# Kernel tuning notes

Measured on AMD Instinct MI355X. Metric: run time of the kernel, lower is better.

The kernel has to match this reference:

```python
import jax, jax.numpy as jnp
import numpy as np

B, C_IN, H, W = 8, 64, 64, 64
C_MID = 32


def setup_inputs() -> dict:
    key = jax.random.key(0)
    ks = jax.random.split(key, 7)
    s = 1.0 / np.sqrt(C_IN)
    return {
        "x": jax.random.normal(ks[0], (B, C_IN, H, W), dtype=jnp.float32),
        "Wk": jax.random.normal(ks[1], (C_MID, C_IN), dtype=jnp.float32) * s,
        "bk": jax.random.normal(ks[2], (C_MID,), dtype=jnp.float32) * 0.01,
        "Wq": jax.random.normal(ks[3], (C_MID, C_IN), dtype=jnp.float32) * s,
        "bq": jax.random.normal(ks[4], (C_MID,), dtype=jnp.float32) * 0.01,
        "Wv": jax.random.normal(ks[5], (C_MID, C_IN), dtype=jnp.float32) * s,
        "bv": jax.random.normal(ks[6], (C_MID,), dtype=jnp.float32) * 0.01,
    }


def reference(x, Wk, bk, Wq, bq, Wv, bv):
    # 1x1 convs == per-pixel channel projections
    def proj(Wt, bt):
        return jnp.einsum('bchw,oc->bohw', x, Wt) + bt[None, :, None, None]

    k = proj(Wk, bk)  # [B, Cm, H, W]
    q = proj(Wq, bq)
    v = proj(Wv, bv)

    b, c, h, w = q.shape
    n = h * w
    qf = q.reshape(b, c, n)
    kf = k.reshape(b, c, n)
    vf = v.reshape(b, c, n)

    # correlated_weight over spatial dims [2,3]: QK channel correlation per
    # pixel pair, softmax over key positions, weighted sum of V.
    scores = jnp.einsum('bcn,bcm->bnm', qf, kf)      # [B, N, N]
    attn = jax.nn.softmax(scores, axis=-1)
    out = jnp.einsum('bnm,bcm->bcn', attn, vf)       # [B, Cm, N]
    return out.reshape(b, c, h, w)
```

## Files before the change

### kernel.cpp

```cpp
#include <hip/hip_runtime.h>
#include <hip/hip_bf16.h>
#include <cstdint>
#include <cstddef>


typedef _Float16 f16x8 __attribute__((ext_vector_type(8)));
typedef float  f32x16 __attribute__((ext_vector_type(16)));
typedef float  f32x4  __attribute__((ext_vector_type(4)));

struct alignas(16) U4 { uint32_t w[4]; };
struct alignas(8)  U2 { uint32_t w[2]; };

#define MFMA16(A, B, C) __builtin_amdgcn_mfma_f32_32x32x16_f16((A), (B), (C), 0, 0, 0)

__device__ __forceinline__ uint16_t f2h(float f) {
    _Float16 h = (_Float16)f;
    return __builtin_bit_cast(uint16_t, h);
}
__device__ __forceinline__ uint32_t cvtpk16(float lo, float hi) {
    auto h2 = __builtin_amdgcn_cvt_pkrtz(lo, hi);
    return __builtin_bit_cast(uint32_t, h2);
}
__device__ __forceinline__ void swp(uint32_t& a, uint32_t& b) {
    asm("v_permlane32_swap_b32 %0, %1" : "+v"(a), "+v"(b));
}
__device__ __forceinline__ float ex2(float x) {
    float r;
    asm("v_exp_f32 %0, %1" : "=v"(r) : "v"(x));
    return r;
}
__device__ __forceinline__ float max3(float a, float b, float c) {
    return fmaxf(fmaxf(a, b), c);
}
__device__ __forceinline__ f16x8 ld8(const void* p) {
    return __builtin_bit_cast(f16x8, *(const U4*)p);
}
__device__ __forceinline__ void gload16(const void* g, void* l) {
    __builtin_amdgcn_global_load_lds(
        (const __attribute__((address_space(1))) void*)g,
        (__attribute__((address_space(3))) void*)l, 16, 0, 0);
}

__global__ __launch_bounds__(256) void proj_kernel(
    const float* __restrict__ x,
    const float* __restrict__ Wk, const float* __restrict__ bk,
    const float* __restrict__ Wq, const float* __restrict__ bq,
    const float* __restrict__ Wv, const float* __restrict__ bv,
    uint16_t* __restrict__ qf, uint16_t* __restrict__ kf,
    uint16_t* __restrict__ vt)
{
    const int g     = blockIdx.x * 256 + threadIdx.x;
    const int pixel = g & 32767;
    const int qt    = __builtin_amdgcn_readfirstlane(g >> 15);
    const int b     = pixel >> 12;
    const int n     = pixel & 4095;
    const int ob    = qt << 2;

    const float* xb = x + (size_t)b * 64 * 4096 + n;
    float xv[64];
    #pragma unroll
    for (int ci = 0; ci < 64; ++ci) xv[ci] = xb[(size_t)ci * 4096];

    #pragma unroll
    for (int pass = 0; pass < 3; ++pass) {
        const float* W    = pass == 0 ? Wk : (pass == 1 ? Wq : Wv);
        const float* bias = pass == 0 ? bk : (pass == 1 ? bq : bv);
        float acc[4];
        #pragma unroll
        for (int o = 0; o < 4; ++o) acc[o] = bias[ob + o];
        #pragma unroll
        for (int o = 0; o < 4; ++o) {
            const float* wr = W + (size_t)(ob + o) * 64;
            #pragma unroll
            for (int ci = 0; ci < 64; ++ci)
                acc[o] = fmaf(wr[ci], xv[ci], acc[o]);
        }
        if (pass == 2) {
            #pragma unroll
            for (int o = 0; o < 4; ++o) {
                int c   = ob + o;
                int nsw = (n & ~0x38) | ((((n >> 3) & 7) ^ (c & 7)) << 3);
                vt[((size_t)(b * 32 + c)) * 4096 + nsw] = f2h(acc[o]);
            }
        } else {
            if (pass == 1) {
                #pragma unroll
                for (int o = 0; o < 4; ++o) acc[o] *= 1.44269504f;
            }
            U2 hp;
            #pragma unroll
            for (int j = 0; j < 2; ++j)
                hp.w[j] = (uint32_t)f2h(acc[2 * j]) | ((uint32_t)f2h(acc[2 * j + 1]) << 16);
            if (pass == 0) {
                char* rowb = (char*)kf + ((size_t)(b * 4096 + n)) * 64;
                *(U2*)(rowb + (((qt >> 1) ^ (n & 3)) * 16) + (qt & 1) * 8) = hp;
            } else {
                uint16_t* hd = qf + ((size_t)(b * 4096 + n)) * 32 + ob;
                *(U2*)hd = hp;
            }
        }
    }
}

__global__ __launch_bounds__(256, 4) void attn_kernel(
    const uint16_t* __restrict__ qf, const uint16_t* __restrict__ kf,
    const uint16_t* __restrict__ vt, float* __restrict__ out,
    float* __restrict__ opart, float* __restrict__ mpart,
    float* __restrict__ lpart, int ns)
{
    __shared__ __align__(16) char lds_k[2][2][4096];
    __shared__ __align__(16) char lds_v[2][2][4096];

    const int blk    = blockIdx.x;
    const int b      = blk & 7;
    const int rest   = blk >> 3;
    const int qblk   = rest & 31;
    const int ksp    = rest >> 5;
    const int ntiles = 64 / ns;
    const int kb0    = ksp * ntiles;
    const int niter  = ntiles >> 1;

    const int tid  = threadIdx.x;
    const int wv   = __builtin_amdgcn_readfirstlane(tid >> 6);
    const int lane = tid & 63;
    const int l31  = lane & 31;
    const int h32  = lane >> 5;
    const int qrow = qblk * 128 + wv * 32 + l31;

    f16x8 q0, q1;
    {
        const uint16_t* r = qf + ((size_t)(b * 4096 + qrow)) * 32;
        q0 = ld8(r + h32 * 8);
        q1 = ld8(r + 16 + h32 * 8);
    }

    f32x16 oacc, zf;
    #pragma unroll
    for (int i = 0; i < 16; ++i) { oacc[i] = 0.f; zf[i] = 0.f; }
    float m_run = -3.0e38f, l_run = 0.f;

    const char* gk   = (const char*)kf + ((size_t)b * 4096) * 64;
    const char* gv   = (const char*)vt
                     + ((size_t)(b * 32 + wv * 8 + (lane >> 3))) * 8192
                     + (lane & 7) * 16;
    const char* gk_l = gk + wv * 1024 + lane * 16;

    const int ka0 = l31 * 64 + ((h32 ^ (l31 & 3)) * 16);
    const int ka1 = l31 * 64 + (((2 + h32) ^ (l31 & 3)) * 16);
    int vo[4];
    #pragma unroll
    for (int j = 0; j < 4; ++j)
        vo[j] = l31 * 128 + (((h32 + 2 * j) ^ (l31 & 7)) * 16);

    gload16(gk_l + (size_t)kb0 * 4096,       lds_k[0][0] + wv * 1024);
    gload16(gv   + (size_t)kb0 * 128,        lds_v[0][0] + wv * 1024);
    gload16(gk_l + (size_t)(kb0 + 1) * 4096, lds_k[0][1] + wv * 1024);
    gload16(gv   + (size_t)(kb0 + 1) * 128,  lds_v[0][1] + wv * 1024);

    int p = 0;
    #pragma unroll 1
    for (int it = 0; it < niter; ++it) {
        __syncthreads();

        if (it + 1 < niter) {
            const int tn = kb0 + 2 * it + 2;
            gload16(gk_l + (size_t)tn * 4096,       lds_k[p ^ 1][0] + wv * 1024);
            gload16(gv   + (size_t)tn * 128,        lds_v[p ^ 1][0] + wv * 1024);
            gload16(gk_l + (size_t)(tn + 1) * 4096, lds_k[p ^ 1][1] + wv * 1024);
            gload16(gv   + (size_t)(tn + 1) * 128,  lds_v[p ^ 1][1] + wv * 1024);
        }

        #pragma unroll
        for (int sl = 0; sl < 2; ++sl) {
            const char* lk = lds_k[p][sl];
            const char* lv = lds_v[p][sl];

            f32x16 s0, s1;
            {
                f16x8 a0 = ld8(lk + ka0);
                f16x8 a1 = ld8(lk + ka1);
                f16x8 c0 = ld8(lk + 2048 + ka0);
                f16x8 c1 = ld8(lk + 2048 + ka1);
                s0 = MFMA16(a0, q0, zf);
                s1 = MFMA16(c0, q0, zf);
                s0 = MFMA16(a1, q1, s0);
                s1 = MFMA16(c1, q1, s1);
            }

            float mx[4];
            #pragma unroll
            for (int i = 0; i < 4; ++i)
                mx[i] = max3(max3(s0[i], s0[i + 4], s0[i + 8]),
                             max3(s0[i + 12], s1[i], s1[i + 4]),
                             fmaxf(s1[i + 8], s1[i + 12]));
            float pm = fmaxf(max3(mx[0], mx[1], mx[2]), mx[3]);
            pm = fmaxf(pm, __shfl_xor(pm, 32));

            if (__any(pm > m_run + 6.f)) {
                float mn  = fmaxf(m_run, pm);
                float scl = ex2(m_run - mn);
                l_run *= scl;
                #pragma unroll
                for (int i = 0; i < 16; ++i) oacc[i] *= scl;
                m_run = mn;
            }

            #pragma unroll
            for (int i = 0; i < 16; ++i) {
                s0[i] = ex2(s0[i] - m_run);
                s1[i] = ex2(s1[i] - m_run);
            }
            float sm[8];
            #pragma unroll
            for (int i = 0; i < 8; ++i)
                sm[i] = (s0[i] + s0[i + 8]) + (s1[i] + s1[i + 8]);
            #pragma unroll
            for (int i = 0; i < 4; ++i) sm[i] += sm[i + 4];
            float rs = (sm[0] + sm[2]) + (sm[1] + sm[3]);
            rs += __shfl_xor(rs, 32);
            l_run += rs;

            U4 f1, f2, f3, f4;
            {
                uint32_t A = cvtpk16(s0[0], s0[1]),  B = cvtpk16(s0[4], s0[5]);   swp(A, B);
                uint32_t C = cvtpk16(s0[2], s0[3]),  D = cvtpk16(s0[6], s0[7]);   swp(C, D);
                f1.w[0] = A; f1.w[1] = C; f1.w[2] = B; f1.w[3] = D;
                A = cvtpk16(s0[8], s0[9]);   B = cvtpk16(s0[12], s0[13]);  swp(A, B);
                C = cvtpk16(s0[10], s0[11]); D = cvtpk16(s0[14], s0[15]);  swp(C, D);
                f2.w[0] = A; f2.w[1] = C; f2.w[2] = B; f2.w[3] = D;
                A = cvtpk16(s1[0], s1[1]);   B = cvtpk16(s1[4], s1[5]);    swp(A, B);
                C = cvtpk16(s1[2], s1[3]);   D = cvtpk16(s1[6], s1[7]);    swp(C, D);
                f3.w[0] = A; f3.w[1] = C; f3.w[2] = B; f3.w[3] = D;
                A = cvtpk16(s1[8], s1[9]);   B = cvtpk16(s1[12], s1[13]);  swp(A, B);
                C = cvtpk16(s1[10], s1[11]); D = cvtpk16(s1[14], s1[15]);  swp(C, D);
                f4.w[0] = A; f4.w[1] = C; f4.w[2] = B; f4.w[3] = D;
            }

            {
                f16x8 v0 = ld8(lv + vo[0]);
                f16x8 v1 = ld8(lv + vo[1]);
                f16x8 v2 = ld8(lv + vo[2]);
                f16x8 v3 = ld8(lv + vo[3]);
                oacc = MFMA16(v0, __builtin_bit_cast(f16x8, f1), oacc);
                oacc = MFMA16(v1, __builtin_bit_cast(f16x8, f2), oacc);
                oacc = MFMA16(v2, __builtin_bit_cast(f16x8, f3), oacc);
                oacc = MFMA16(v3, __builtin_bit_cast(f16x8, f4), oacc);
            }
        }
        p ^= 1;
    }

    if (ns == 1) {
        const float inv = 1.f / l_run;
        float* ob = out + ((size_t)b * 32) * 4096 + qrow;
        #pragma unroll
        for (int i = 0; i < 16; ++i) {
            int c = (i & 3) + 8 * (i >> 2) + 4 * h32;
            ob[(size_t)c * 4096] = oacc[i] * inv;
        }
    } else {
        float* op = opart + ((size_t)((ksp * 8 + b) * 32)) * 4096 + qrow;
        #pragma unroll
        for (int i = 0; i < 16; ++i) {
            int c = (i & 3) + 8 * (i >> 2) + 4 * h32;
            op[(size_t)c * 4096] = oacc[i];
        }
        if (h32 == 0) {
            mpart[((size_t)(ksp * 8 + b)) * 4096 + qrow] = m_run;
            lpart[((size_t)(ksp * 8 + b)) * 4096 + qrow] = l_run;
        }
    }
}

__global__ __launch_bounds__(256) void reduce_kernel(
    const float* __restrict__ opart, const float* __restrict__ mpart,
    const float* __restrict__ lpart, float* __restrict__ out, int ns)
{
    const int idx = blockIdx.x * 256 + threadIdx.x;
    const int nq  = idx & 1023;
    const int c   = (idx >> 10) & 31;
    const int b   = idx >> 15;
    const size_t noff = (size_t)nq * 4;

    f32x4 M;
    #pragma unroll
    for (int e = 0; e < 4; ++e) M[e] = -3.0e38f;
    for (int s = 0; s < ns; ++s) {
        f32x4 mm = *(const f32x4*)(mpart + ((size_t)(s * 8 + b)) * 4096 + noff);
        #pragma unroll
        for (int e = 0; e < 4; ++e) M[e] = fmaxf(M[e], mm[e]);
    }
    f32x4 L, O;
    #pragma unroll
    for (int e = 0; e < 4; ++e) { L[e] = 0.f; O[e] = 0.f; }
    for (int s = 0; s < ns; ++s) {
        f32x4 mm = *(const f32x4*)(mpart + ((size_t)(s * 8 + b)) * 4096 + noff);
        f32x4 ll = *(const f32x4*)(lpart + ((size_t)(s * 8 + b)) * 4096 + noff);
        f32x4 oo = *(const f32x4*)(opart + ((size_t)((s * 8 + b) * 32 + c)) * 4096 + noff);
        #pragma unroll
        for (int e = 0; e < 4; ++e) {
            float w = ex2(mm[e] - M[e]);
            L[e] += ll[e] * w;
            O[e] += oo[e] * w;
        }
    }
    f32x4 r;
    #pragma unroll
    for (int e = 0; e < 4; ++e) r[e] = O[e] / L[e];
    *(f32x4*)(out + ((size_t)(b * 32 + c)) * 4096 + noff) = r;
}

extern "C" void kernel_launch(void* const* d_in, const int* in_sizes, int n_in,
                              void* d_out, int out_size, void* d_ws, size_t ws_size,
                              hipStream_t stream)
{
    (void)in_sizes; (void)n_in; (void)out_size;
    const float* x  = (const float*)d_in[0];
    const float* Wk = (const float*)d_in[1];
    const float* bk = (const float*)d_in[2];
    const float* Wq = (const float*)d_in[3];
    const float* bq = (const float*)d_in[4];
    const float* Wv = (const float*)d_in[5];
    const float* bv = (const float*)d_in[6];
    float* out = (float*)d_out;

    char* ws = (char*)d_ws;
    const size_t SZ = (size_t)8 * 4096 * 32 * 2;
    uint16_t* qf = (uint16_t*)(ws);
    uint16_t* kf = (uint16_t*)(ws + SZ);
    uint16_t* vt = (uint16_t*)(ws + 2 * SZ);
    const size_t base = 3 * SZ;

    const size_t OB  = (size_t)8 * 32 * 4096 * 4;
    const size_t MB_ = (size_t)8 * 4096 * 4;
    int ns = 1;
    if      (ws_size >= base + 4 * (OB + 2 * MB_)) ns = 4;
    else if (ws_size >= base + 2 * (OB + 2 * MB_)) ns = 2;

    float* opart = (float*)(ws + base);
    float* mpart = (float*)(ws + base + (size_t)ns * OB);
    float* lpart = (float*)(ws + base + (size_t)ns * OB + (size_t)ns * MB_);

    proj_kernel<<<1024, 256, 0, stream>>>(x, Wk, bk, Wq, bq, Wv, bv,
                                          qf, kf, vt);
    attn_kernel<<<ns * 256, 256, 0, stream>>>(qf, kf, vt, out,
                                              opart, mpart, lpart, ns);
    if (ns > 1)
        reduce_kernel<<<1024, 256, 0, stream>>>(opart, mpart, lpart, out, ns);
}
```

Before: 62.31 us.

## Widen projection work per thread and store split-K partials as bf16

The projection kernel now computes 16 output channels per thread instead of 4. That cuts the grid from 1024 to 256 blocks, so each thread reloads its 64 input values four times fewer, and Q/K get written with 16-byte stores. The split-K partial outputs are stored as bf16 instead of fp32, which halves the partial-buffer traffic between the attention and reduce kernels. The costs are fewer projection blocks with more registers each (less parallelism) and lower precision in the partial sums.

```diff
diff --git a/kernel.cpp b/kernel.cpp
--- a/kernel.cpp
+++ b/kernel.cpp
@@ -16,6 +16,15 @@
 __device__ __forceinline__ uint16_t f2h(float f) {
     _Float16 h = (_Float16)f;
     return __builtin_bit_cast(uint16_t, h);
+}
+__device__ __forceinline__ uint16_t f2bf(float f) {
+    uint32_t u = __builtin_bit_cast(uint32_t, f);
+    u += 0x7fffu + ((u >> 16) & 1u);
+    return (uint16_t)(u >> 16);
+}
+__device__ __forceinline__ float bf2f(uint32_t h16) {
+    uint32_t u = h16 << 16;
+    return __builtin_bit_cast(float, u);
 }
 __device__ __forceinline__ uint32_t cvtpk16(float lo, float hi) {
     auto h2 = __builtin_amdgcn_cvt_pkrtz(lo, hi);
@@ -51,10 +60,10 @@
 {
     const int g     = blockIdx.x * 256 + threadIdx.x;
     const int pixel = g & 32767;
-    const int qt    = __builtin_amdgcn_readfirstlane(g >> 15);
+    const int half  = __builtin_amdgcn_readfirstlane(g >> 15);
     const int b     = pixel >> 12;
     const int n     = pixel & 4095;
-    const int ob    = qt << 2;
+    const int ob    = half << 4;
 
     const float* xb = x + (size_t)b * 64 * 4096 + n;
     float xv[64];
@@ -65,11 +74,11 @@
     for (int pass = 0; pass < 3; ++pass) {
         const float* W    = pass == 0 ? Wk : (pass == 1 ? Wq : Wv);
         const float* bias = pass == 0 ? bk : (pass == 1 ? bq : bv);
-        float acc[4];
-        #pragma unroll
-        for (int o = 0; o < 4; ++o) acc[o] = bias[ob + o];
-        #pragma unroll
-        for (int o = 0; o < 4; ++o) {
+        float acc[16];
+        #pragma unroll
+        for (int o = 0; o < 16; ++o) acc[o] = bias[ob + o];
+        #pragma unroll
+        for (int o = 0; o < 16; ++o) {
             const float* wr = W + (size_t)(ob + o) * 64;
             #pragma unroll
             for (int ci = 0; ci < 64; ++ci)
@@ -77,7 +86,7 @@
         }
         if (pass == 2) {
             #pragma unroll
-            for (int o = 0; o < 4; ++o) {
+            for (int o = 0; o < 16; ++o) {
                 int c   = ob + o;
                 int nsw = (n & ~0x38) | ((((n >> 3) & 7) ^ (c & 7)) << 3);
                 vt[((size_t)(b * 32 + c)) * 4096 + nsw] = f2h(acc[o]);
@@ -85,18 +94,22 @@
         } else {
             if (pass == 1) {
                 #pragma unroll
-                for (int o = 0; o < 4; ++o) acc[o] *= 1.44269504f;
-            }
-            U2 hp;
-            #pragma unroll
-            for (int j = 0; j < 2; ++j)
-                hp.w[j] = (uint32_t)f2h(acc[2 * j]) | ((uint32_t)f2h(acc[2 * j + 1]) << 16);
+                for (int o = 0; o < 16; ++o) acc[o] *= 1.44269504f;
+            }
+            U4 u0, u1;
+            #pragma unroll
+            for (int t = 0; t < 4; ++t) {
+                u0.w[t] = (uint32_t)f2h(acc[2 * t])     | ((uint32_t)f2h(acc[2 * t + 1]) << 16);
+                u1.w[t] = (uint32_t)f2h(acc[8 + 2 * t]) | ((uint32_t)f2h(acc[8 + 2 * t + 1]) << 16);
+            }
             if (pass == 0) {
                 char* rowb = (char*)kf + ((size_t)(b * 4096 + n)) * 64;
-                *(U2*)(rowb + (((qt >> 1) ^ (n & 3)) * 16) + (qt & 1) * 8) = hp;
+                *(U4*)(rowb + (((2 * half)     ^ (n & 3)) * 16)) = u0;
+                *(U4*)(rowb + (((2 * half + 1) ^ (n & 3)) * 16)) = u1;
             } else {
                 uint16_t* hd = qf + ((size_t)(b * 4096 + n)) * 32 + ob;
-                *(U2*)hd = hp;
+                *(U4*)hd       = u0;
+                *(U4*)(hd + 8) = u1;
             }
         }
     }
@@ -105,7 +118,7 @@
 __global__ __launch_bounds__(256, 4) void attn_kernel(
     const uint16_t* __restrict__ qf, const uint16_t* __restrict__ kf,
     const uint16_t* __restrict__ vt, float* __restrict__ out,
-    float* __restrict__ opart, float* __restrict__ mpart,
+    uint16_t* __restrict__ opart, float* __restrict__ mpart,
     float* __restrict__ lpart, int ns)
 {
     __shared__ __align__(16) char lds_k[2][2][4096];
@@ -259,11 +272,11 @@
             ob[(size_t)c * 4096] = oacc[i] * inv;
         }
     } else {
-        float* op = opart + ((size_t)((ksp * 8 + b) * 32)) * 4096 + qrow;
+        uint16_t* op = opart + ((size_t)((ksp * 8 + b) * 32)) * 4096 + qrow;
         #pragma unroll
         for (int i = 0; i < 16; ++i) {
             int c = (i & 3) + 8 * (i >> 2) + 4 * h32;
-            op[(size_t)c * 4096] = oacc[i];
+            op[(size_t)c * 4096] = f2bf(oacc[i]);
         }
         if (h32 == 0) {
             mpart[((size_t)(ksp * 8 + b)) * 4096 + qrow] = m_run;
@@ -273,7 +286,7 @@
 }
 
 __global__ __launch_bounds__(256) void reduce_kernel(
-    const float* __restrict__ opart, const float* __restrict__ mpart,
+    const uint16_t* __restrict__ opart, const float* __restrict__ mpart,
     const float* __restrict__ lpart, float* __restrict__ out, int ns)
 {
     const int idx = blockIdx.x * 256 + threadIdx.x;
@@ -296,12 +309,17 @@
     for (int s = 0; s < ns; ++s) {
         f32x4 mm = *(const f32x4*)(mpart + ((size_t)(s * 8 + b)) * 4096 + noff);
         f32x4 ll = *(const f32x4*)(lpart + ((size_t)(s * 8 + b)) * 4096 + noff);
-        f32x4 oo = *(const f32x4*)(opart + ((size_t)((s * 8 + b) * 32 + c)) * 4096 + noff);
+        U2 uu = *(const U2*)(opart + ((size_t)((s * 8 + b) * 32 + c)) * 4096 + noff);
+        float ov[4];
+        ov[0] = bf2f(uu.w[0] & 0xffffu);
+        ov[1] = bf2f(uu.w[0] >> 16);
+        ov[2] = bf2f(uu.w[1] & 0xffffu);
+        ov[3] = bf2f(uu.w[1] >> 16);
         #pragma unroll
         for (int e = 0; e < 4; ++e) {
             float w = ex2(mm[e] - M[e]);
             L[e] += ll[e] * w;
-            O[e] += oo[e] * w;
+            O[e] += ov[e] * w;
         }
     }
     f32x4 r;
@@ -331,18 +349,18 @@
     uint16_t* vt = (uint16_t*)(ws + 2 * SZ);
     const size_t base = 3 * SZ;
 
-    const size_t OB  = (size_t)8 * 32 * 4096 * 4;
+    const size_t OB  = (size_t)8 * 32 * 4096 * 2;
     const size_t MB_ = (size_t)8 * 4096 * 4;
     int ns = 1;
     if      (ws_size >= base + 4 * (OB + 2 * MB_)) ns = 4;
     else if (ws_size >= base + 2 * (OB + 2 * MB_)) ns = 2;
 
-    float* opart = (float*)(ws + base);
-    float* mpart = (float*)(ws + base + (size_t)ns * OB);
-    float* lpart = (float*)(ws + base + (size_t)ns * OB + (size_t)ns * MB_);
-
-    proj_kernel<<<1024, 256, 0, stream>>>(x, Wk, bk, Wq, bq, Wv, bv,
-                                          qf, kf, vt);
+    uint16_t* opart = (uint16_t*)(ws + base);
+    float*    mpart = (float*)(ws + base + (size_t)ns * OB);
+    float*    lpart = (float*)(ws + base + (size_t)ns * OB + (size_t)ns * MB_);
+
+    proj_kernel<<<256, 256, 0, stream>>>(x, Wk, bk, Wq, bq, Wv, bv,
+                                         qf, kf, vt);
     attn_kernel<<<ns * 256, 256, 0, stream>>>(qf, kf, vt, out,
                                               opart, mpart, lpart, ns);
     if (ns > 1)
```

New measurement: 74.50 us. 19.6% more time.
